# Optimization experiments

Measured on AMD Instinct MI355X. Metric: run time of the kernel, lower is better.

Reference implementation:

```python
import jax, jax.numpy as jnp
import numpy as np

N_EMBD = 2048
HEAD_DIM = 128
N_CTX = 2048
BATCH = 8
SEQ = 2048


def setup_inputs() -> dict:
    key = jax.random.key(0)
    ks = jax.random.split(key, 7)
    s = 1.0 / np.sqrt(N_EMBD)
    x = jax.random.normal(ks[0], (BATCH, SEQ, N_EMBD), dtype=jnp.float32)
    # torch Linear params: weight (out, in), bias (out,)
    Wq = jax.random.uniform(ks[1], (HEAD_DIM, N_EMBD), jnp.float32, -s, s)
    bq = jax.random.uniform(ks[2], (HEAD_DIM,), jnp.float32, -s, s)
    Wk = jax.random.uniform(ks[3], (HEAD_DIM, N_EMBD), jnp.float32, -s, s)
    bk = jax.random.uniform(ks[4], (HEAD_DIM,), jnp.float32, -s, s)
    Wv = jax.random.uniform(ks[5], (HEAD_DIM, N_EMBD), jnp.float32, -s, s)
    bv = jax.random.uniform(ks[6], (HEAD_DIM,), jnp.float32, -s, s)
    return {"x": x, "Wq": Wq, "bq": bq, "Wk": Wk, "bk": bk, "Wv": Wv, "bv": bv}


def reference(x, Wq, bq, Wk, bk, Wv, bv):
    # projections: y = x @ W^T + b
    q = jnp.einsum('bse,de->bsd', x, Wq) + bq  # (B, S, D)
    k = jnp.einsum('bse,de->bsd', x, Wk) + bk
    v = jnp.einsum('bse,de->bsd', x, Wv) + bv
    seq = x.shape[1]
    scores = jnp.einsum('bqd,bkd->bqk', q, k)  # (B, S, S)
    # causal mask: strictly-upper-triangular positions set to -inf (before scaling, as in source)
    causal = jnp.triu(jnp.ones((seq, seq), dtype=bool), k=1)
    scores = jnp.where(causal[None, :, :], -jnp.inf, scores)
    # NOTE: source scales by sqrt(seq_size), not sqrt(head_dim)
    weight = jax.nn.softmax(scores / jnp.sqrt(jnp.float32(seq)), axis=-1)
    return jnp.einsum('bqk,bkd->bqd', weight, v)
```

## Files before the change

### kernel.cpp

```cpp
#include <hip/hip_runtime.h>
#include <cmath>

#define BATCH 8
#define SEQ   2048
#define NEMB  2048
#define HD    128
#define NROWS (BATCH * SEQ)

typedef __bf16 v8bf __attribute__((ext_vector_type(8)));
typedef float  f32x4 __attribute__((ext_vector_type(4)));

union U8 { v8bf v; __bf16 b[8]; unsigned short e[8]; };

__device__ inline void async16(void* lds, const void* g) {
  __builtin_amdgcn_global_load_lds(
      (const __attribute__((address_space(1))) unsigned int*)g,
      (__attribute__((address_space(3))) unsigned int*)lds, 16, 0, 0);
}

__device__ inline v8bf cvt8(float4 a, float4 b) {
  U8 u;
  u.b[0] = (__bf16)a.x; u.b[1] = (__bf16)a.y; u.b[2] = (__bf16)a.z; u.b[3] = (__bf16)a.w;
  u.b[4] = (__bf16)b.x; u.b[5] = (__bf16)b.y; u.b[6] = (__bf16)b.z; u.b[7] = (__bf16)b.w;
  return u.v;
}

__global__ __launch_bounds__(256) void wconv_kernel(
    const float* __restrict__ Wq, const float* __restrict__ Wk,
    const float* __restrict__ Wv, __bf16* __restrict__ out) {
  const int id = blockIdx.x;
  const int proj = id >> 6, blk = id & 63;
  const float* __restrict__ W = proj == 0 ? Wq : proj == 1 ? Wk : Wv;
  __bf16* __restrict__ o = out + (size_t)proj * (HD * NEMB);
  const int base = blk * 4096 + threadIdx.x * 16;
  const float4* s = (const float4*)(W + base);
  float4 f0 = s[0], f1 = s[1], f2 = s[2], f3 = s[3];
  *(v8bf*)(o + base) = cvt8(f0, f1);
  *(v8bf*)(o + base + 8) = cvt8(f2, f3);
}

__global__ __launch_bounds__(256, 3) void qkv_proj_kernel(
    const float* __restrict__ x, const __bf16* __restrict__ Wb,
    const float* __restrict__ bq, const float* __restrict__ bk,
    const float* __restrict__ bv,
    __bf16* __restrict__ Qb, __bf16* __restrict__ Kb, __bf16* __restrict__ Vb)
{
  const int bid0 = blockIdx.x;
  const int bid = ((bid0 & 7) * 96) + (bid0 >> 3);
  const int mt = bid / 3;
  const int proj = bid % 3;
  const __bf16* __restrict__ W = Wb + (size_t)proj * (HD * NEMB);
  const float* __restrict__ bias = proj == 0 ? bq : proj == 1 ? bk : bv;
  __bf16* __restrict__ Out = proj == 0 ? Qb : proj == 1 ? Kb : Vb;
  const int m0 = mt * 64;

  __shared__ __bf16 Asm[64 * 128];
  __shared__ __bf16 Bsm[128 * 128];

  const int t = threadIdx.x, lane = t & 63, w = t >> 6;
  const int wm = w >> 1, wn = w & 1;
  const int hi = lane >> 4, lo = lane & 15;

  const float* pa[4];
  int aw[4];
#pragma unroll
  for (int i = 0; i < 4; ++i) {
    const int r = (w * 4 + i) * 4 + (lane >> 4);
    const int p = lane & 15;
    pa[i] = x + (size_t)(m0 + r) * NEMB + p * 8;
    aw[i] = r * 256 + ((p ^ (r & 7)) << 4);
  }
  const __bf16* pb[8];
  char* lb[8];
#pragma unroll
  for (int i = 0; i < 8; ++i) {
    const int j = w * 8 + i;
    const int r = j * 4 + (lane >> 4);
    const int c = (lane & 15) ^ (r & 7);
    pb[i] = W + (size_t)r * NEMB + c * 8;
    lb[i] = (char*)Bsm + j * 1024;
  }

  f32x4 acc[2][4];
  const f32x4 fz = {0.f, 0.f, 0.f, 0.f};
#pragma unroll
  for (int m = 0; m < 2; ++m)
#pragma unroll
    for (int n = 0; n < 4; ++n) acc[m][n] = fz;

  float4 fa[4][2];
  auto ALOAD = [&](int tt) {
#pragma unroll
    for (int i = 0; i < 4; ++i) {
      const float* p = pa[i] + tt * 128;
      fa[i][0] = *(const float4*)(p);
      fa[i][1] = *(const float4*)(p + 4);
    }
  };
  auto AWRITE = [&]() {
#pragma unroll
    for (int i = 0; i < 4; ++i)
      *(v8bf*)((char*)Asm + aw[i]) = cvt8(fa[i][0], fa[i][1]);
  };
  auto STAGE_B = [&](int tt) {
#pragma unroll
    for (int i = 0; i < 8; ++i) async16(lb[i], pb[i] + tt * 128);
  };

  const int NT = NEMB / 128;
  ALOAD(0);
  for (int tt = 0; tt < NT; ++tt) {
    __syncthreads();
    STAGE_B(tt);
    AWRITE();
    __syncthreads();
    if (tt + 1 < NT) ALOAD(tt + 1);

#pragma unroll
    for (int kk = 0; kk < 4; ++kk) {
      const int kc = kk * 4 + hi;
      v8bf a[2], b[4];
#pragma unroll
      for (int m = 0; m < 2; ++m) {
        const int r = wm * 32 + m * 16 + lo;
        a[m] = *(const v8bf*)((const char*)Asm + r * 256 + ((kc ^ (r & 7)) << 4));
      }
#pragma unroll
      for (int n = 0; n < 4; ++n) {
        const int r = wn * 64 + n * 16 + lo;
        b[n] = *(const v8bf*)((const char*)Bsm + r * 256 + ((kc ^ (r & 7)) << 4));
      }
#pragma unroll
      for (int m = 0; m < 2; ++m)
#pragma unroll
        for (int n = 0; n < 4; ++n)
          acc[m][n] = __builtin_amdgcn_mfma_f32_16x16x32_bf16(a[m], b[n], acc[m][n], 0, 0, 0);
    }
  }

#pragma unroll
  for (int n = 0; n < 4; ++n) {
    const int col = wn * 64 + n * 16 + lo;
    const float bi = bias[col];
#pragma unroll
    for (int m = 0; m < 2; ++m) {
#pragma unroll
      for (int r = 0; r < 4; ++r) {
        const int row = m0 + wm * 32 + m * 16 + hi * 4 + r;
        Out[(size_t)row * HD + col] = (__bf16)(acc[m][n][r] + bi);
      }
    }
  }
}

__global__ __launch_bounds__(256) void attn_kernel(
    const __bf16* __restrict__ Qb, const __bf16* __restrict__ Kb,
    const __bf16* __restrict__ Vb, __bf16* __restrict__ Opart,
    float* __restrict__ Ml)
{
  const int bid0 = blockIdx.x;
  const int bid = ((bid0 & 7) << 7) + (bid0 >> 3);
  const int b = bid >> 7;
  const int q = bid & 127;
  const int qt = q >> 2;
  const int s  = q & 3;
  const int q0 = qt * 64;
  const int kv_beg = (s * (qt + 1)) >> 2;
  const int kv_end = ((s + 1) * (qt + 1)) >> 2;
  const int nst = kv_end - kv_beg;

  const int t = threadIdx.x, lane = t & 63, w = t >> 6;
  const int hi = lane >> 4, lo = lane & 15;

  __shared__ __bf16 Ksm[2][64 * 128];
  __shared__ __bf16 Vtsm[2][128 * 64];
  __shared__ __bf16 Psm[4][16 * 64];

  v8bf aQ[4];
  {
    const __bf16* qp = Qb + ((size_t)(b * SEQ + q0 + w * 16 + lo)) * HD + hi * 8;
#pragma unroll
    for (int kk = 0; kk < 4; ++kk) aQ[kk] = *(const v8bf*)(qp + kk * 32);
  }

  const __bf16* kga[4];
#pragma unroll
  for (int i = 0; i < 4; ++i) {
    const int r = (w * 4 + i) * 4 + (lane >> 4);
    const int c = (lane & 15) ^ (r & 7);
    kga[i] = Kb + ((size_t)(b * SEQ) + r) * HD + c * 8;
  }

  const int keyg = t >> 4, dg = t & 15;
  U8 vv[4];

  f32x4 accO[8];
  const f32x4 fz = {0.f, 0.f, 0.f, 0.f};
#pragma unroll
  for (int n = 0; n < 8; ++n) accO[n] = fz;
  float m_s[4], l_s[4];
#pragma unroll
  for (int r = 0; r < 4; ++r) { m_s[r] = -INFINITY; l_s[r] = 0.f; }

  const float scale = 0.022097086912079608f;

  if (nst > 0) {
    auto STAGE_K = [&](int kv, int buf) {
      const size_t off = (size_t)kv * 64 * HD;
      char* kb = (char*)&Ksm[buf][0];
#pragma unroll
      for (int i = 0; i < 4; ++i) async16(kb + (w * 4 + i) * 1024, kga[i] + off);
    };
    auto LOAD_V = [&](int kv) {
      const __bf16* vp = Vb + ((size_t)(b * SEQ + kv * 64 + keyg * 4)) * HD + dg * 8;
#pragma unroll
      for (int j = 0; j < 4; ++j) vv[j].v = *(const v8bf*)(vp + (size_t)j * HD);
    };
    auto WRITE_VT = [&](int buf) {
      char* vb2 = (char*)&Vtsm[buf][0];
#pragma unroll
      for (int dd = 0; dd < 8; ++dd) {
        const int d = (dd + dg) & 7;
        ushort4 pk = make_ushort4(vv[0].e[d], vv[1].e[d], vv[2].e[d], vv[3].e[d]);
        const int row = dg * 8 + d;
        *(ushort4*)(vb2 + row * 128 + ((keyg * 8) ^ ((row & 7) << 4))) = pk;
      }
    };

    STAGE_K(kv_beg, 0);
    LOAD_V(kv_beg);
    WRITE_VT(0);
    __syncthreads();

    for (int t2 = 0; t2 < nst; ++t2) {
      const int kv = kv_beg + t2;
      const int cur = t2 & 1;
      const bool more = (t2 + 1 < nst);
      if (more) { STAGE_K(kv + 1, cur ^ 1); LOAD_V(kv + 1); }

      f32x4 accS[4];
#pragma unroll
      for (int n = 0; n < 4; ++n) accS[n] = fz;
      const char* ksm = (const char*)&Ksm[cur][0];
#pragma unroll
      for (int kk = 0; kk < 4; ++kk) {
        const int cb = kk * 64 + hi * 16;
        v8bf bk[4];
#pragma unroll
        for (int n = 0; n < 4; ++n) {
          const int r = n * 16 + lo;
          bk[n] = *(const v8bf*)(ksm + r * 256 + (cb ^ ((r & 7) << 4)));
        }
#pragma unroll
        for (int n = 0; n < 4; ++n)
          accS[n] = __builtin_amdgcn_mfma_f32_16x16x32_bf16(aQ[kk], bk[n], accS[n], 0, 0, 0);
      }

      float sv[4][4];
      const bool diag = (kv == qt);
#pragma unroll
      for (int n = 0; n < 4; ++n)
#pragma unroll
        for (int r = 0; r < 4; ++r) {
          float v = accS[n][r] * scale;
          if (diag) {
            const int key = kv * 64 + n * 16 + lo;
            const int qr = q0 + w * 16 + hi * 4 + r;
            if (key > qr) v = -INFINITY;
          }
          sv[n][r] = v;
        }

      float mx[4];
#pragma unroll
      for (int r = 0; r < 4; ++r) {
        mx[r] = fmaxf(fmaxf(sv[0][r], sv[1][r]), fmaxf(sv[2][r], sv[3][r]));
#pragma unroll
        for (int off = 1; off < 16; off <<= 1)
          mx[r] = fmaxf(mx[r], __shfl_xor(mx[r], off));
      }
      float corr[4], p[4][4], rs[4];
#pragma unroll
      for (int r = 0; r < 4; ++r) {
        const float mnew = fmaxf(m_s[r], mx[r]);
        corr[r] = __expf(m_s[r] - mnew);
        m_s[r] = mnew;
        rs[r] = 0.f;
      }
#pragma unroll
      for (int n = 0; n < 4; ++n)
#pragma unroll
        for (int r = 0; r < 4; ++r) {
          p[n][r] = __expf(sv[n][r] - m_s[r]);
          rs[r] += p[n][r];
        }
#pragma unroll
      for (int r = 0; r < 4; ++r) {
#pragma unroll
        for (int off = 1; off < 16; off <<= 1) rs[r] += __shfl_xor(rs[r], off);
        l_s[r] = l_s[r] * corr[r] + rs[r];
      }
#pragma unroll
      for (int n = 0; n < 8; ++n)
#pragma unroll
        for (int r = 0; r < 4; ++r) accO[n][r] *= corr[r];

#pragma unroll
      for (int n = 0; n < 4; ++n)
#pragma unroll
        for (int r = 0; r < 4; ++r) {
          const int row = hi * 4 + r;
          __bf16 h = (__bf16)p[n][r];
          *(unsigned short*)((char*)&Psm[w][0] + row * 128 +
                             (((n * 16 + lo) * 2) ^ ((row & 7) << 4))) =
              __builtin_bit_cast(unsigned short, h);
        }

      if (more) WRITE_VT(cur ^ 1);

      const char* vsm = (const char*)&Vtsm[cur][0];
#pragma unroll
      for (int k2 = 0; k2 < 2; ++k2) {
        const int cb = k2 * 64 + hi * 16;
        const v8bf aP = *(const v8bf*)((const char*)&Psm[w][0] + lo * 128 + (cb ^ ((lo & 7) << 4)));
#pragma unroll
        for (int n = 0; n < 8; ++n) {
          const int r = n * 16 + lo;
          const v8bf bv = *(const v8bf*)(vsm + r * 128 + (cb ^ ((r & 7) << 4)));
          accO[n] = __builtin_amdgcn_mfma_f32_16x16x32_bf16(aP, bv, accO[n], 0, 0, 0);
        }
      }
      if (more) __syncthreads();
    }
  }

#pragma unroll
  for (int r = 0; r < 4; ++r) {
    const int qr = q0 + w * 16 + hi * 4 + r;
    __bf16* op = Opart + ((size_t)s * NROWS + b * SEQ + qr) * HD + lo;
#pragma unroll
    for (int n = 0; n < 8; ++n) op[n * 16] = (__bf16)accO[n][r];
    if (lo == 0) {
      float* mlp = Ml + ((size_t)s * NROWS + b * SEQ + qr) * 2;
      mlp[0] = m_s[r];
      mlp[1] = l_s[r];
    }
  }
}

__global__ __launch_bounds__(256) void combine_kernel(
    const __bf16* __restrict__ Opart, const float* __restrict__ Ml,
    float* __restrict__ out)
{
  const int idx = blockIdx.x * 256 + threadIdx.x;
  const int row = idx >> 2, ch = idx & 3;
  float m[4], l[4];
#pragma unroll
  for (int s = 0; s < 4; ++s) {
    const float* mlp = Ml + ((size_t)s * NROWS + row) * 2;
    m[s] = mlp[0];
    l[s] = mlp[1];
  }
  const float M = fmaxf(fmaxf(m[0], m[1]), fmaxf(m[2], m[3]));
  float e[4], denom = 0.f;
#pragma unroll
  for (int s = 0; s < 4; ++s) { e[s] = __expf(m[s] - M); denom += l[s] * e[s]; }
  const float inv = 1.f / denom;

  float* po = out + (size_t)row * HD + ch * 32;
#pragma unroll
  for (int j = 0; j < 4; ++j) {
    float sum[8];
#pragma unroll
    for (int q2 = 0; q2 < 8; ++q2) sum[q2] = 0.f;
#pragma unroll
    for (int s = 0; s < 4; ++s) {
      U8 o;
      o.v = *(const v8bf*)(Opart + ((size_t)s * NROWS + row) * HD + ch * 32 + j * 8);
#pragma unroll
      for (int q2 = 0; q2 < 8; ++q2) sum[q2] += (float)o.b[q2] * e[s];
    }
#pragma unroll
    for (int q2 = 0; q2 < 8; ++q2) po[j * 8 + q2] = sum[q2] * inv;
  }
}

extern "C" void kernel_launch(void* const* d_in, const int* in_sizes, int n_in,
                              void* d_out, int out_size, void* d_ws, size_t ws_size,
                              hipStream_t stream) {
  const float* x  = (const float*)d_in[0];
  const float* Wq = (const float*)d_in[1];
  const float* bq = (const float*)d_in[2];
  const float* Wk = (const float*)d_in[3];
  const float* bk = (const float*)d_in[4];
  const float* Wv = (const float*)d_in[5];
  const float* bv = (const float*)d_in[6];
  float* out = (float*)d_out;

  __bf16* Qb = (__bf16*)d_ws;
  __bf16* Kb = Qb + (size_t)NROWS * HD;
  __bf16* Vb = Kb + (size_t)NROWS * HD;
  __bf16* Wb = Vb + (size_t)NROWS * HD;
  __bf16* Opart = Wb + (size_t)3 * HD * NEMB;
  float*  Ml = (float*)(Opart + (size_t)4 * NROWS * HD);

  wconv_kernel<<<dim3(3 * 64), dim3(256), 0, stream>>>(Wq, Wk, Wv, Wb);
  qkv_proj_kernel<<<dim3(256 * 3), dim3(256), 0, stream>>>(
      x, Wb, bq, bk, bv, Qb, Kb, Vb);
  attn_kernel<<<dim3(BATCH * 32 * 4), dim3(256), 0, stream>>>(Qb, Kb, Vb, Opart, Ml);
  combine_kernel<<<dim3(NROWS * 4 / 256), dim3(256), 0, stream>>>(Opart, Ml, out);
}
```

Before: 116.7 us.

## Fuse Q/K/V projections into one block per row tile with async double buffering

Each block now computes all three projections for a 64-row tile, so x is read from global memory once instead of three times. x tiles are staged as fp32 straight into LDS with async global-to-LDS loads and converted to bf16 at fragment-read time. The K loop uses a two-stage LDS double buffer with explicit vmcnt waits, so loads overlap with MFMA work. The cost is 512-thread blocks, 128KB of shared memory, only 256 blocks (low occupancy), and extra per-fragment conversion ALU work.

Measured after the change: 111.3 us, median of 2. 1.05x faster.

```diff
diff --git a/kernel.cpp b/kernel.cpp
--- a/kernel.cpp
+++ b/kernel.cpp
@@ -11,6 +11,7 @@
 typedef float  f32x4 __attribute__((ext_vector_type(4)));
 
 union U8 { v8bf v; __bf16 b[8]; unsigned short e[8]; };
+union F4 { f32x4 v; float f[4]; };
 
 __device__ inline void async16(void* lds, const void* g) {
   __builtin_amdgcn_global_load_lds(
@@ -39,108 +40,122 @@
   *(v8bf*)(o + base + 8) = cvt8(f2, f3);
 }
 
-__global__ __launch_bounds__(256, 3) void qkv_proj_kernel(
+__global__ __launch_bounds__(512) void qkv_fused_kernel(
     const float* __restrict__ x, const __bf16* __restrict__ Wb,
     const float* __restrict__ bq, const float* __restrict__ bk,
     const float* __restrict__ bv,
     __bf16* __restrict__ Qb, __bf16* __restrict__ Kb, __bf16* __restrict__ Vb)
 {
   const int bid0 = blockIdx.x;
-  const int bid = ((bid0 & 7) * 96) + (bid0 >> 3);
-  const int mt = bid / 3;
-  const int proj = bid % 3;
-  const __bf16* __restrict__ W = Wb + (size_t)proj * (HD * NEMB);
-  const float* __restrict__ bias = proj == 0 ? bq : proj == 1 ? bk : bv;
-  __bf16* __restrict__ Out = proj == 0 ? Qb : proj == 1 ? Kb : Vb;
+  const int mt = ((bid0 & 7) << 5) + (bid0 >> 3);
   const int m0 = mt * 64;
 
-  __shared__ __bf16 Asm[64 * 128];
-  __shared__ __bf16 Bsm[128 * 128];
+  __shared__ char smem[131072];
+  char* const A0 = smem;
+  char* const A1 = smem + 16384;
+  char* const Bu0 = smem + 32768;
+  char* const Bu1 = smem + 81920;
 
   const int t = threadIdx.x, lane = t & 63, w = t >> 6;
-  const int wm = w >> 1, wn = w & 1;
+  const int wm = w >> 2, wn4 = w & 3;
   const int hi = lane >> 4, lo = lane & 15;
 
-  const float* pa[4];
-  int aw[4];
-#pragma unroll
-  for (int i = 0; i < 4; ++i) {
-    const int r = (w * 4 + i) * 4 + (lane >> 4);
-    const int p = lane & 15;
-    pa[i] = x + (size_t)(m0 + r) * NEMB + p * 8;
-    aw[i] = r * 256 + ((p ^ (r & 7)) << 4);
-  }
-  const __bf16* pb[8];
-  char* lb[8];
-#pragma unroll
-  for (int i = 0; i < 8; ++i) {
-    const int j = w * 8 + i;
+  const float* pa[2];
+  int laOff[2];
+#pragma unroll
+  for (int i = 0; i < 2; ++i) {
+    const int j = w * 2 + i;
     const int r = j * 4 + (lane >> 4);
     const int c = (lane & 15) ^ (r & 7);
-    pb[i] = W + (size_t)r * NEMB + c * 8;
-    lb[i] = (char*)Bsm + j * 1024;
-  }
-
-  f32x4 acc[2][4];
+    pa[i] = x + (size_t)(m0 + r) * NEMB + c * 4;
+    laOff[i] = j * 1024;
+  }
+  const __bf16* pb[6];
+  int lbOff[6];
+#pragma unroll
+  for (int i = 0; i < 6; ++i) {
+    const int j = w * 6 + i;
+    const int r = j * 8 + (lane >> 3);
+    const int pj = r >> 7, wr = r & 127;
+    const int c = (lane & 7) ^ (r & 7);
+    pb[i] = Wb + (size_t)pj * (HD * NEMB) + (size_t)wr * NEMB + c * 8;
+    lbOff[i] = j * 1024;
+  }
+
+  f32x4 acc[2][6];
   const f32x4 fz = {0.f, 0.f, 0.f, 0.f};
 #pragma unroll
   for (int m = 0; m < 2; ++m)
 #pragma unroll
-    for (int n = 0; n < 4; ++n) acc[m][n] = fz;
-
-  float4 fa[4][2];
-  auto ALOAD = [&](int tt) {
-#pragma unroll
-    for (int i = 0; i < 4; ++i) {
-      const float* p = pa[i] + tt * 128;
-      fa[i][0] = *(const float4*)(p);
-      fa[i][1] = *(const float4*)(p + 4);
-    }
+    for (int n = 0; n < 6; ++n) acc[m][n] = fz;
+
+  auto STAGE = [&](int tt, char* Ab, char* Bb) {
+    const int k0 = tt * 64;
+#pragma unroll
+    for (int i = 0; i < 2; ++i) async16(Ab + laOff[i], pa[i] + k0);
+#pragma unroll
+    for (int i = 0; i < 6; ++i) async16(Bb + lbOff[i], pb[i] + k0);
   };
-  auto AWRITE = [&]() {
-#pragma unroll
-    for (int i = 0; i < 4; ++i)
-      *(v8bf*)((char*)Asm + aw[i]) = cvt8(fa[i][0], fa[i][1]);
-  };
-  auto STAGE_B = [&](int tt) {
-#pragma unroll
-    for (int i = 0; i < 8; ++i) async16(lb[i], pb[i] + tt * 128);
-  };
-
-  const int NT = NEMB / 128;
-  ALOAD(0);
-  for (int tt = 0; tt < NT; ++tt) {
-    __syncthreads();
-    STAGE_B(tt);
-    AWRITE();
-    __syncthreads();
-    if (tt + 1 < NT) ALOAD(tt + 1);
-
-#pragma unroll
-    for (int kk = 0; kk < 4; ++kk) {
-      const int kc = kk * 4 + hi;
-      v8bf a[2], b[4];
+  auto COMPUTE = [&](const char* Ab, const char* Bb) {
+#pragma unroll
+    for (int kk = 0; kk < 2; ++kk) {
+      v8bf a[2], b[6];
 #pragma unroll
       for (int m = 0; m < 2; ++m) {
         const int r = wm * 32 + m * 16 + lo;
-        a[m] = *(const v8bf*)((const char*)Asm + r * 256 + ((kc ^ (r & 7)) << 4));
-      }
-#pragma unroll
-      for (int n = 0; n < 4; ++n) {
-        const int r = wn * 64 + n * 16 + lo;
-        b[n] = *(const v8bf*)((const char*)Bsm + r * 256 + ((kc ^ (r & 7)) << 4));
+        const int s = kk * 8 + hi * 2;
+        const char* rowp = Ab + r * 256;
+        F4 a0, a1;
+        a0.v = *(const f32x4*)(rowp + (((s)     ^ (r & 7)) << 4));
+        a1.v = *(const f32x4*)(rowp + (((s + 1) ^ (r & 7)) << 4));
+        U8 u;
+#pragma unroll
+        for (int q = 0; q < 4; ++q) {
+          u.b[q]     = (__bf16)a0.f[q];
+          u.b[q + 4] = (__bf16)a1.f[q];
+        }
+        a[m] = u.v;
+      }
+      const int kc = kk * 4 + hi;
+#pragma unroll
+      for (int n = 0; n < 6; ++n) {
+        const int r = wn4 * 96 + n * 16 + lo;
+        b[n] = *(const v8bf*)(Bb + r * 128 + ((kc ^ (r & 7)) << 4));
       }
 #pragma unroll
       for (int m = 0; m < 2; ++m)
 #pragma unroll
-        for (int n = 0; n < 4; ++n)
+        for (int n = 0; n < 6; ++n)
           acc[m][n] = __builtin_amdgcn_mfma_f32_16x16x32_bf16(a[m], b[n], acc[m][n], 0, 0, 0);
     }
-  }
-
-#pragma unroll
-  for (int n = 0; n < 4; ++n) {
-    const int col = wn * 64 + n * 16 + lo;
+  };
+
+  const int NT = NEMB / 64;
+  STAGE(0, A0, Bu0);
+  for (int tt = 0; tt < NT; tt += 2) {
+    __builtin_amdgcn_s_barrier();
+    STAGE(tt + 1, A1, Bu1);
+    asm volatile("s_waitcnt vmcnt(8)" ::: "memory");
+    __builtin_amdgcn_s_barrier();
+    COMPUTE(A0, Bu0);
+    __builtin_amdgcn_s_barrier();
+    if (tt + 2 < NT) {
+      STAGE(tt + 2, A0, Bu0);
+      asm volatile("s_waitcnt vmcnt(8)" ::: "memory");
+    } else {
+      asm volatile("s_waitcnt vmcnt(0)" ::: "memory");
+    }
+    __builtin_amdgcn_s_barrier();
+    COMPUTE(A1, Bu1);
+  }
+
+#pragma unroll
+  for (int n = 0; n < 6; ++n) {
+    const int rrb = wn4 * 96 + n * 16;
+    const int pj = rrb >> 7;
+    const int col = (rrb & 127) + lo;
+    __bf16* __restrict__ Out = pj == 0 ? Qb : pj == 1 ? Kb : Vb;
+    const float* __restrict__ bias = pj == 0 ? bq : pj == 1 ? bk : bv;
     const float bi = bias[col];
 #pragma unroll
     for (int m = 0; m < 2; ++m) {
@@ -405,7 +420,7 @@
   float*  Ml = (float*)(Opart + (size_t)4 * NROWS * HD);
 
   wconv_kernel<<<dim3(3 * 64), dim3(256), 0, stream>>>(Wq, Wk, Wv, Wb);
-  qkv_proj_kernel<<<dim3(256 * 3), dim3(256), 0, stream>>>(
+  qkv_fused_kernel<<<dim3(256), dim3(512), 0, stream>>>(
       x, Wb, bq, bk, bv, Qb, Kb, Vb);
   attn_kernel<<<dim3(BATCH * 32 * 4), dim3(256), 0, stream>>>(Qb, Kb, Vb, Opart, Ml);
   combine_kernel<<<dim3(NROWS * 4 / 256), dim3(256), 0, stream>>>(Opart, Ml, out);
```

## Pre-pack x and W into MFMA fragment layout and drop LDS staging

Applied to the files above, without the earlier changes.

Adds xpack and wpack kernels that convert x and the weights to bf16 and store them in the exact per-lane MFMA fragment order. The QKV projection GEMM then loads fragments straight from global memory into registers, double-buffered across k-steps, with no shared memory and no __syncthreads. This removes LDS staging, barriers and the in-loop fp32 to bf16 conversion. In exchange it adds a full extra pass that writes a bf16 copy of x, and it loses operand sharing between the waves of a block, so more global/L2 traffic is spent on redundant fragment loads.

Result: slower. 143.7 us (+23.1%).

```diff
diff --git a/kernel.cpp b/kernel.cpp
--- a/kernel.cpp
+++ b/kernel.cpp
@@ -25,22 +25,42 @@
   return u.v;
 }
 
-__global__ __launch_bounds__(256) void wconv_kernel(
+__global__ __launch_bounds__(256) void xpack_kernel(
+    const float* __restrict__ x, __bf16* __restrict__ xp) {
+  const int g = blockIdx.x * 256 + threadIdx.x;
+  const int lane = g & 63;
+  const int u = g >> 6;
+  const int kk = u & 1;
+  const int fm = (u >> 1) & 3;
+  const int tt = (u >> 3) & 31;
+  const int mt = u >> 8;
+  const int row = mt * 64 + fm * 16 + (lane & 15);
+  const int k   = tt * 64 + kk * 32 + (lane >> 4) * 8;
+  const float4* s = (const float4*)(x + (size_t)row * NEMB + k);
+  float4 f0 = s[0], f1 = s[1];
+  *(v8bf*)(xp + (size_t)g * 8) = cvt8(f0, f1);
+}
+
+__global__ __launch_bounds__(256) void wpack_kernel(
     const float* __restrict__ Wq, const float* __restrict__ Wk,
-    const float* __restrict__ Wv, __bf16* __restrict__ out) {
-  const int id = blockIdx.x;
-  const int proj = id >> 6, blk = id & 63;
-  const float* __restrict__ W = proj == 0 ? Wq : proj == 1 ? Wk : Wv;
-  __bf16* __restrict__ o = out + (size_t)proj * (HD * NEMB);
-  const int base = blk * 4096 + threadIdx.x * 16;
-  const float4* s = (const float4*)(W + base);
-  float4 f0 = s[0], f1 = s[1], f2 = s[2], f3 = s[3];
-  *(v8bf*)(o + base) = cvt8(f0, f1);
-  *(v8bf*)(o + base + 8) = cvt8(f2, f3);
-}
-
-__global__ __launch_bounds__(256, 3) void qkv_proj_kernel(
-    const float* __restrict__ x, const __bf16* __restrict__ Wb,
+    const float* __restrict__ Wv, __bf16* __restrict__ wp) {
+  const int g = blockIdx.x * 256 + threadIdx.x;
+  const int lane = g & 63;
+  const int u = g >> 6;
+  const int kk = u & 1;
+  const int tt = (u >> 1) & 31;
+  const int nf = (u >> 6) & 7;
+  const int p  = u >> 9;
+  const float* __restrict__ W = p == 0 ? Wq : p == 1 ? Wk : Wv;
+  const int row = nf * 16 + (lane & 15);
+  const int k   = tt * 64 + kk * 32 + (lane >> 4) * 8;
+  const float4* s = (const float4*)(W + (size_t)row * NEMB + k);
+  float4 f0 = s[0], f1 = s[1];
+  *(v8bf*)(wp + (size_t)g * 8) = cvt8(f0, f1);
+}
+
+__global__ __launch_bounds__(256) void qkv_proj_kernel(
+    const __bf16* __restrict__ xp, const __bf16* __restrict__ wp,
     const float* __restrict__ bq, const float* __restrict__ bk,
     const float* __restrict__ bv,
     __bf16* __restrict__ Qb, __bf16* __restrict__ Kb, __bf16* __restrict__ Vb)
@@ -49,37 +69,15 @@
   const int bid = ((bid0 & 7) * 96) + (bid0 >> 3);
   const int mt = bid / 3;
   const int proj = bid % 3;
-  const __bf16* __restrict__ W = Wb + (size_t)proj * (HD * NEMB);
   const float* __restrict__ bias = proj == 0 ? bq : proj == 1 ? bk : bv;
   __bf16* __restrict__ Out = proj == 0 ? Qb : proj == 1 ? Kb : Vb;
-  const int m0 = mt * 64;
-
-  __shared__ __bf16 Asm[64 * 128];
-  __shared__ __bf16 Bsm[128 * 128];
 
   const int t = threadIdx.x, lane = t & 63, w = t >> 6;
   const int wm = w >> 1, wn = w & 1;
   const int hi = lane >> 4, lo = lane & 15;
 
-  const float* pa[4];
-  int aw[4];
-#pragma unroll
-  for (int i = 0; i < 4; ++i) {
-    const int r = (w * 4 + i) * 4 + (lane >> 4);
-    const int p = lane & 15;
-    pa[i] = x + (size_t)(m0 + r) * NEMB + p * 8;
-    aw[i] = r * 256 + ((p ^ (r & 7)) << 4);
-  }
-  const __bf16* pb[8];
-  char* lb[8];
-#pragma unroll
-  for (int i = 0; i < 8; ++i) {
-    const int j = w * 8 + i;
-    const int r = j * 4 + (lane >> 4);
-    const int c = (lane & 15) ^ (r & 7);
-    pb[i] = W + (size_t)r * NEMB + c * 8;
-    lb[i] = (char*)Bsm + j * 1024;
-  }
+  const __bf16* abase = xp + (size_t)(mt * 32) * 4096 + lane * 8;
+  const __bf16* bbase = wp + (size_t)(proj * 8 + wn * 4) * 32768 + lane * 8;
 
   f32x4 acc[2][4];
   const f32x4 fz = {0.f, 0.f, 0.f, 0.f};
@@ -88,54 +86,38 @@
 #pragma unroll
     for (int n = 0; n < 4; ++n) acc[m][n] = fz;
 
-  float4 fa[4][2];
-  auto ALOAD = [&](int tt) {
-#pragma unroll
-    for (int i = 0; i < 4; ++i) {
-      const float* p = pa[i] + tt * 128;
-      fa[i][0] = *(const float4*)(p);
-      fa[i][1] = *(const float4*)(p + 4);
-    }
+  v8bf A0[2][2], A1[2][2];
+  v8bf B0[4][2], B1[4][2];
+
+  auto LD = [&](v8bf (&A)[2][2], v8bf (&B)[4][2], int tt) {
+#pragma unroll
+    for (int m = 0; m < 2; ++m)
+#pragma unroll
+      for (int kk = 0; kk < 2; ++kk)
+        A[m][kk] = *(const v8bf*)(abase + (size_t)(tt * 8 + (wm * 2 + m) * 2 + kk) * 512);
+#pragma unroll
+    for (int n = 0; n < 4; ++n)
+#pragma unroll
+      for (int kk = 0; kk < 2; ++kk)
+        B[n][kk] = *(const v8bf*)(bbase + (size_t)(n * 64 + tt * 2 + kk) * 512);
   };
-  auto AWRITE = [&]() {
-#pragma unroll
-    for (int i = 0; i < 4; ++i)
-      *(v8bf*)((char*)Asm + aw[i]) = cvt8(fa[i][0], fa[i][1]);
+  auto STEP = [&](v8bf (&A)[2][2], v8bf (&B)[4][2]) {
+#pragma unroll
+    for (int kk = 0; kk < 2; ++kk)
+#pragma unroll
+      for (int m = 0; m < 2; ++m)
+#pragma unroll
+        for (int n = 0; n < 4; ++n)
+          acc[m][n] = __builtin_amdgcn_mfma_f32_16x16x32_bf16(A[m][kk], B[n][kk], acc[m][n], 0, 0, 0);
   };
-  auto STAGE_B = [&](int tt) {
-#pragma unroll
-    for (int i = 0; i < 8; ++i) async16(lb[i], pb[i] + tt * 128);
-  };
-
-  const int NT = NEMB / 128;
-  ALOAD(0);
-  for (int tt = 0; tt < NT; ++tt) {
-    __syncthreads();
-    STAGE_B(tt);
-    AWRITE();
-    __syncthreads();
-    if (tt + 1 < NT) ALOAD(tt + 1);
-
-#pragma unroll
-    for (int kk = 0; kk < 4; ++kk) {
-      const int kc = kk * 4 + hi;
-      v8bf a[2], b[4];
-#pragma unroll
-      for (int m = 0; m < 2; ++m) {
-        const int r = wm * 32 + m * 16 + lo;
-        a[m] = *(const v8bf*)((const char*)Asm + r * 256 + ((kc ^ (r & 7)) << 4));
-      }
-#pragma unroll
-      for (int n = 0; n < 4; ++n) {
-        const int r = wn * 64 + n * 16 + lo;
-        b[n] = *(const v8bf*)((const char*)Bsm + r * 256 + ((kc ^ (r & 7)) << 4));
-      }
-#pragma unroll
-      for (int m = 0; m < 2; ++m)
-#pragma unroll
-        for (int n = 0; n < 4; ++n)
-          acc[m][n] = __builtin_amdgcn_mfma_f32_16x16x32_bf16(a[m], b[n], acc[m][n], 0, 0, 0);
-    }
+
+  const int NT = NEMB / 64;
+  LD(A0, B0, 0);
+  for (int tt = 0; tt < NT; tt += 2) {
+    LD(A1, B1, tt + 1);
+    STEP(A0, B0);
+    if (tt + 2 < NT) LD(A0, B0, tt + 2);
+    STEP(A1, B1);
   }
 
 #pragma unroll
@@ -146,7 +128,7 @@
     for (int m = 0; m < 2; ++m) {
 #pragma unroll
       for (int r = 0; r < 4; ++r) {
-        const int row = m0 + wm * 32 + m * 16 + hi * 4 + r;
+        const int row = mt * 64 + wm * 32 + m * 16 + hi * 4 + r;
         Out[(size_t)row * HD + col] = (__bf16)(acc[m][n][r] + bi);
       }
     }
@@ -400,13 +382,15 @@
   __bf16* Qb = (__bf16*)d_ws;
   __bf16* Kb = Qb + (size_t)NROWS * HD;
   __bf16* Vb = Kb + (size_t)NROWS * HD;
-  __bf16* Wb = Vb + (size_t)NROWS * HD;
-  __bf16* Opart = Wb + (size_t)3 * HD * NEMB;
+  __bf16* Wp = Vb + (size_t)NROWS * HD;
+  __bf16* Xp = Wp + (size_t)1536 * 512;
+  __bf16* Opart = Xp + (size_t)65536 * 512;
   float*  Ml = (float*)(Opart + (size_t)4 * NROWS * HD);
 
-  wconv_kernel<<<dim3(3 * 64), dim3(256), 0, stream>>>(Wq, Wk, Wv, Wb);
+  wpack_kernel<<<dim3(384), dim3(256), 0, stream>>>(Wq, Wk, Wv, Wp);
+  xpack_kernel<<<dim3(16384), dim3(256), 0, stream>>>(x, Xp);
   qkv_proj_kernel<<<dim3(256 * 3), dim3(256), 0, stream>>>(
-      x, Wb, bq, bk, bv, Qb, Kb, Vb);
+      Xp, Wp, bq, bk, bv, Qb, Kb, Vb);
   attn_kernel<<<dim3(BATCH * 32 * 4), dim3(256), 0, stream>>>(Qb, Kb, Vb, Opart, Ml);
   combine_kernel<<<dim3(NROWS * 4 / 256), dim3(256), 0, stream>>>(Opart, Ml, out);
 }
```

## Stage fp32 x via async LDS loads and enlarge projection M-tile to 128

Applied to the files above, without the earlier changes.

The QKV projection now copies fp32 x tiles straight into LDS with global_load_lds and converts them to bf16 when reading fragments, instead of loading into registers and converting before the LDS store. The M tile grows from 64 to 128 rows with a K tile of 64, so each block does 4x4 MFMA tiles per wave and half as many blocks launch. This removes the register staging and conversion of A from the load path and reuses each W tile across more rows. In exchange it drops the register prefetch overlap, converts each A element once per N-wave (twice per element), and runs twice as many K iterations, each with two barriers.

Result: no change. 116.8 us (+0.0%).

```diff
diff --git a/kernel.cpp b/kernel.cpp
--- a/kernel.cpp
+++ b/kernel.cpp
@@ -11,6 +11,7 @@
 typedef float  f32x4 __attribute__((ext_vector_type(4)));
 
 union U8 { v8bf v; __bf16 b[8]; unsigned short e[8]; };
+union F4 { f32x4 v; float f[4]; };
 
 __device__ inline void async16(void* lds, const void* g) {
   __builtin_amdgcn_global_load_lds(
@@ -46,92 +47,85 @@
     __bf16* __restrict__ Qb, __bf16* __restrict__ Kb, __bf16* __restrict__ Vb)
 {
   const int bid0 = blockIdx.x;
-  const int bid = ((bid0 & 7) * 96) + (bid0 >> 3);
+  const int bid = ((bid0 & 7) * 48) + (bid0 >> 3);
   const int mt = bid / 3;
   const int proj = bid % 3;
   const __bf16* __restrict__ W = Wb + (size_t)proj * (HD * NEMB);
   const float* __restrict__ bias = proj == 0 ? bq : proj == 1 ? bk : bv;
   __bf16* __restrict__ Out = proj == 0 ? Qb : proj == 1 ? Kb : Vb;
-  const int m0 = mt * 64;
-
-  __shared__ __bf16 Asm[64 * 128];
-  __shared__ __bf16 Bsm[128 * 128];
+  const int m0 = mt * 128;
+
+  __shared__ float  Asm[128 * 64];
+  __shared__ __bf16 Bsm[128 * 64];
 
   const int t = threadIdx.x, lane = t & 63, w = t >> 6;
   const int wm = w >> 1, wn = w & 1;
   const int hi = lane >> 4, lo = lane & 15;
 
-  const float* pa[4];
-  int aw[4];
-#pragma unroll
-  for (int i = 0; i < 4; ++i) {
-    const int r = (w * 4 + i) * 4 + (lane >> 4);
-    const int p = lane & 15;
-    pa[i] = x + (size_t)(m0 + r) * NEMB + p * 8;
-    aw[i] = r * 256 + ((p ^ (r & 7)) << 4);
-  }
-  const __bf16* pb[8];
-  char* lb[8];
+  const float* pa[8];
+  char* la[8];
 #pragma unroll
   for (int i = 0; i < 8; ++i) {
     const int j = w * 8 + i;
     const int r = j * 4 + (lane >> 4);
     const int c = (lane & 15) ^ (r & 7);
+    pa[i] = x + (size_t)(m0 + r) * NEMB + c * 4;
+    la[i] = (char*)Asm + j * 1024;
+  }
+  const __bf16* pb[4];
+  char* lb[4];
+#pragma unroll
+  for (int i = 0; i < 4; ++i) {
+    const int j = w * 4 + i;
+    const int r = j * 8 + (lane >> 3);
+    const int c = (lane & 7) ^ (r & 7);
     pb[i] = W + (size_t)r * NEMB + c * 8;
     lb[i] = (char*)Bsm + j * 1024;
   }
 
-  f32x4 acc[2][4];
+  f32x4 acc[4][4];
   const f32x4 fz = {0.f, 0.f, 0.f, 0.f};
 #pragma unroll
-  for (int m = 0; m < 2; ++m)
+  for (int m = 0; m < 4; ++m)
 #pragma unroll
     for (int n = 0; n < 4; ++n) acc[m][n] = fz;
 
-  float4 fa[4][2];
-  auto ALOAD = [&](int tt) {
-#pragma unroll
-    for (int i = 0; i < 4; ++i) {
-      const float* p = pa[i] + tt * 128;
-      fa[i][0] = *(const float4*)(p);
-      fa[i][1] = *(const float4*)(p + 4);
-    }
-  };
-  auto AWRITE = [&]() {
-#pragma unroll
-    for (int i = 0; i < 4; ++i)
-      *(v8bf*)((char*)Asm + aw[i]) = cvt8(fa[i][0], fa[i][1]);
-  };
-  auto STAGE_B = [&](int tt) {
-#pragma unroll
-    for (int i = 0; i < 8; ++i) async16(lb[i], pb[i] + tt * 128);
-  };
-
-  const int NT = NEMB / 128;
-  ALOAD(0);
-  for (int tt = 0; tt < NT; ++tt) {
+  for (int tt = 0; tt < NEMB / 64; ++tt) {
+    const int k0 = tt * 64;
     __syncthreads();
-    STAGE_B(tt);
-    AWRITE();
+#pragma unroll
+    for (int i = 0; i < 8; ++i) async16(la[i], pa[i] + k0);
+#pragma unroll
+    for (int i = 0; i < 4; ++i) async16(lb[i], pb[i] + k0);
     __syncthreads();
-    if (tt + 1 < NT) ALOAD(tt + 1);
-
-#pragma unroll
-    for (int kk = 0; kk < 4; ++kk) {
-      const int kc = kk * 4 + hi;
-      v8bf a[2], b[4];
-#pragma unroll
-      for (int m = 0; m < 2; ++m) {
-        const int r = wm * 32 + m * 16 + lo;
-        a[m] = *(const v8bf*)((const char*)Asm + r * 256 + ((kc ^ (r & 7)) << 4));
+
+#pragma unroll
+    for (int kk = 0; kk < 2; ++kk) {
+      v8bf a[4], b[4];
+#pragma unroll
+      for (int m = 0; m < 4; ++m) {
+        const int r = wm * 64 + m * 16 + lo;
+        const int s = kk * 8 + hi * 2;
+        const char* rowp = (const char*)Asm + r * 256;
+        F4 a0, a1;
+        a0.v = *(const f32x4*)(rowp + (((s)     ^ (r & 7)) << 4));
+        a1.v = *(const f32x4*)(rowp + (((s + 1) ^ (r & 7)) << 4));
+        U8 u;
+#pragma unroll
+        for (int q = 0; q < 4; ++q) {
+          u.b[q]     = (__bf16)a0.f[q];
+          u.b[q + 4] = (__bf16)a1.f[q];
+        }
+        a[m] = u.v;
       }
 #pragma unroll
       for (int n = 0; n < 4; ++n) {
         const int r = wn * 64 + n * 16 + lo;
-        b[n] = *(const v8bf*)((const char*)Bsm + r * 256 + ((kc ^ (r & 7)) << 4));
-      }
-#pragma unroll
-      for (int m = 0; m < 2; ++m)
+        const int kc = kk * 4 + hi;
+        b[n] = *(const v8bf*)((const char*)Bsm + r * 128 + ((kc ^ (r & 7)) << 4));
+      }
+#pragma unroll
+      for (int m = 0; m < 4; ++m)
 #pragma unroll
         for (int n = 0; n < 4; ++n)
           acc[m][n] = __builtin_amdgcn_mfma_f32_16x16x32_bf16(a[m], b[n], acc[m][n], 0, 0, 0);
@@ -143,10 +137,10 @@
     const int col = wn * 64 + n * 16 + lo;
     const float bi = bias[col];
 #pragma unroll
-    for (int m = 0; m < 2; ++m) {
+    for (int m = 0; m < 4; ++m) {
 #pragma unroll
       for (int r = 0; r < 4; ++r) {
-        const int row = m0 + wm * 32 + m * 16 + hi * 4 + r;
+        const int row = m0 + wm * 64 + m * 16 + hi * 4 + r;
         Out[(size_t)row * HD + col] = (__bf16)(acc[m][n][r] + bi);
       }
     }
@@ -405,7 +399,7 @@
   float*  Ml = (float*)(Opart + (size_t)4 * NROWS * HD);
 
   wconv_kernel<<<dim3(3 * 64), dim3(256), 0, stream>>>(Wq, Wk, Wv, Wb);
-  qkv_proj_kernel<<<dim3(256 * 3), dim3(256), 0, stream>>>(
+  qkv_proj_kernel<<<dim3(128 * 3), dim3(256), 0, stream>>>(
       x, Wb, bq, bk, bv, Qb, Kb, Vb);
   attn_kernel<<<dim3(BATCH * 32 * 4), dim3(256), 0, stream>>>(Qb, Kb, Vb, Opart, Ml);
   combine_kernel<<<dim3(NROWS * 4 / 256), dim3(256), 0, stream>>>(Opart, Ml, out);
```
